# Kernel optimization log

Hardware: AMD Instinct MI355X
Metric: run time of the kernel (lower is better)

## Reference

```python
import jax, jax.numpy as jnp
import numpy as np
import math

B, WIN, C_IN, C_OUT = 8, 512, 38, 38
D_MODEL, N_HEADS, E_LAYERS, D_FF = 512, 8, 3, 512
EH = D_MODEL // N_HEADS
LN_EPS = 1e-3  # keras LayerNormalization default


def setup_inputs() -> dict:
    key = jax.random.key(0)
    ks = jax.random.split(key, 24)
    s = 0.02
    rn = lambda k, sh: jax.random.normal(k, sh, jnp.float32) * s
    L, d, H = E_LAYERS, D_MODEL, N_HEADS
    return {
        "x": jax.random.normal(ks[0], (B, WIN, C_IN), jnp.float32),
        "conv_k": rn(ks[1], (3, C_IN, d)),
        "Wq": rn(ks[2], (L, d, d)), "bq": jnp.zeros((L, d), jnp.float32),
        "Wk": rn(ks[3], (L, d, d)), "bk": jnp.zeros((L, d), jnp.float32),
        "Wv": rn(ks[4], (L, d, d)), "bv": jnp.zeros((L, d), jnp.float32),
        "Ws": rn(ks[5], (L, d, H)), "bs": jnp.zeros((L, H), jnp.float32),
        "Wo": rn(ks[6], (L, d, d)), "bo": jnp.zeros((L, d), jnp.float32),
        "W1": rn(ks[7], (L, d, D_FF)), "b1": jnp.zeros((L, D_FF), jnp.float32),
        "W2": rn(ks[8], (L, D_FF, d)), "b2": jnp.zeros((L, d), jnp.float32),
        "ln1_g": jnp.ones((L, d), jnp.float32), "ln1_b": jnp.zeros((L, d), jnp.float32),
        "ln2_g": jnp.ones((L, d), jnp.float32), "ln2_b": jnp.zeros((L, d), jnp.float32),
        "lnf_g": jnp.ones((d,), jnp.float32), "lnf_b": jnp.zeros((d,), jnp.float32),
        "Wp": rn(ks[9], (d, C_OUT)), "bp": jnp.zeros((C_OUT,), jnp.float32),
    }


def _layernorm(x, g, b):
    mu = jnp.mean(x, axis=-1, keepdims=True)
    var = jnp.mean((x - mu) ** 2, axis=-1, keepdims=True)
    return (x - mu) * jax.lax.rsqrt(var + LN_EPS) * g + b


def _pos_embedding():
    pos = jnp.arange(WIN, dtype=jnp.float32)[:, None]
    div = jnp.exp(jnp.arange(0, D_MODEL, 2, dtype=jnp.float32) * (-math.log(10000.0) / D_MODEL))
    # interleave sin at even idx, cos at odd idx
    return jnp.stack([jnp.sin(pos * div), jnp.cos(pos * div)], axis=-1).reshape(WIN, D_MODEL)


def reference(x, conv_k, Wq, bq, Wk, bk, Wv, bv, Ws, bs, Wo, bo,
              W1, b1, W2, b2, ln1_g, ln1_b, ln2_g, ln2_b, lnf_g, lnf_b, Wp, bp):
    # --- DataEmbedding: wrap-pad then Conv1D(k=3, valid), plus sinusoidal PE ---
    xp = jnp.concatenate([x[:, -1:], x, x[:, :1]], axis=1)
    h = jax.lax.conv_general_dilated(xp, conv_k, window_strides=(1,), padding='VALID',
                                     dimension_numbers=('NWC', 'WIO', 'NWC'))
    h = h + _pos_embedding()[None]

    idx = jnp.arange(WIN, dtype=jnp.float32)
    dist = jnp.abs(idx[:, None] - idx[None, :])
    scale = 1.0 / math.sqrt(EH)
    inv_sqrt_2pi = 1.0 / math.sqrt(2.0 * math.pi)

    series_l, prior_l, sigma_l = [], [], []
    for i in range(E_LAYERS):
        q = (h @ Wq[i] + bq[i]).reshape(B, WIN, N_HEADS, EH)
        k = (h @ Wk[i] + bk[i]).reshape(B, WIN, N_HEADS, EH)
        v = (h @ Wv[i] + bv[i]).reshape(B, WIN, N_HEADS, EH)
        sig = h @ Ws[i] + bs[i]

        scores = jnp.einsum('blhe,bshe->bhls', q, k)  # mask_flag=False in model
        series = jax.nn.softmax(scores * scale, axis=-1)  # [B, H, L, S]

        sg = jnp.transpose(sig, (0, 2, 1))               # [B, H, L]
        sg = jax.nn.sigmoid(sg * 5.0) + 1e-5
        sg = jnp.power(3.0, sg) - 1.0
        sg4 = jnp.broadcast_to(sg[..., None], (B, N_HEADS, WIN, WIN))
        prior = inv_sqrt_2pi / sg4 * jnp.exp(-(dist ** 2) / (2.0 * sg4 ** 2))

        attn_out = jnp.einsum('bhls,bshd->blhd', series, v).reshape(B, WIN, D_MODEL)
        h = _layernorm(h + attn_out @ Wo[i] + bo[i], ln1_g[i], ln1_b[i])
        y = jax.nn.gelu(h @ W1[i] + b1[i], approximate=False)
        y = y @ W2[i] + b2[i]
        h = _layernorm(h + y, ln2_g[i], ln2_b[i])

        series_l.append(series); prior_l.append(prior); sigma_l.append(sg4)

    h = _layernorm(h, lnf_g, lnf_b)
    out = h @ Wp + bp
    return (out, jnp.stack(series_l), jnp.stack(prior_l), jnp.stack(sigma_l))
```

## Files before the change

### kernel.cpp

```cpp
#include <hip/hip_runtime.h>
#include <math.h>


typedef unsigned short ushort;
typedef __attribute__((ext_vector_type(8))) ushort ushort8;
typedef __attribute__((ext_vector_type(8))) short short8;
typedef __attribute__((ext_vector_type(4))) float float4v;

__device__ inline ushort f2bf(float f) {
  union { float f; unsigned u; } v; v.f = f;
  return (ushort)((v.u + 0x7fffu + ((v.u >> 16) & 1u)) >> 16);
}

__device__ inline void gload16(const void* g, void* l) {
  __builtin_amdgcn_global_load_lds(
      (const __attribute__((address_space(1))) unsigned int*)g,
      (__attribute__((address_space(3))) unsigned int*)l, 16, 0, 0);
}

__global__ __launch_bounds__(512) void embed_kernel(const float* __restrict__ x,
                                                    const float* __restrict__ ck,
                                                    float* __restrict__ h,
                                                    ushort* __restrict__ hb) {
  int bt = blockIdx.x;
  int b = bt >> 9, t = bt & 511;
  int co = threadIdx.x;
  __shared__ float xs[3][38];
  if (co < 114) {
    int w = co / 38, ci = co - w * 38;
    int r = (t - 1 + w + 512) & 511;
    xs[w][ci] = x[((long)(b << 9) + r) * 38 + ci];
  }
  __syncthreads();
  float acc = 0.f;
#pragma unroll
  for (int w = 0; w < 3; ++w)
#pragma unroll
    for (int ci = 0; ci < 38; ++ci)
      acc = fmaf(xs[w][ci], ck[(w * 38 + ci) * 512 + co], acc);
  float div = expf((float)(co & ~1) * (-9.210340371976184f / 512.f));
  float ang = (float)t * div;
  float pe = (co & 1) ? cosf(ang) : sinf(ang);
  float o = acc + pe;
  h[(long)bt * 512 + co] = o;
  hb[(long)bt * 512 + co] = f2bf(o);
}

__global__ __launch_bounds__(256) void wcvt_kernel(const float* __restrict__ W,
                                                   ushort* __restrict__ Wt,
                                                   long lstride) {
  int l = blockIdx.z;
  int n = blockIdx.x * 256 + threadIdx.x;
  int k0 = blockIdx.y * 8;
  const float* w = W + (long)l * 262144;
  ushort* o = Wt + (long)l * lstride;
  ushort8 v;
#pragma unroll
  for (int i = 0; i < 8; ++i) v[i] = f2bf(w[(long)(k0 + i) * 512 + n]);
  *(ushort8*)&o[(long)n * 512 + k0] = v;
}

__global__ __launch_bounds__(512) void bcat_kernel(const float* __restrict__ bq,
                                                   const float* __restrict__ bk,
                                                   const float* __restrict__ bv,
                                                   float* __restrict__ bqkv) {
  int l = blockIdx.x, t = threadIdx.x;
  bqkv[l * 1536 + t] = bq[l * 512 + t];
  bqkv[l * 1536 + 512 + t] = bk[l * 512 + t];
  bqkv[l * 1536 + 1024 + t] = bv[l * 512 + t];
}

template <bool GELU_, bool CBF16>
__global__ __launch_bounds__(256) void gemm_bt(
    const ushort* __restrict__ A, int lda,
    const ushort* __restrict__ B, int ldb,
    const float* __restrict__ bias,
    void* __restrict__ Cv, int ldc, int K) {
  __shared__ ushort As[4096];
  __shared__ ushort Bs[2048];
  int t = threadIdx.x;
  int m0 = blockIdx.y * 128, n0 = blockIdx.x * 64;
  int w = t >> 6, lane = t & 63;
  int wr = (w >> 1) * 64, wc = (w & 1) * 32;
  int fm = lane & 15, q4 = lane >> 4;
  float4v acc[4][2];
#pragma unroll
  for (int i = 0; i < 4; ++i)
#pragma unroll
    for (int j = 0; j < 2; ++j) acc[i][j] = (float4v){0.f, 0.f, 0.f, 0.f};

  int kk = (lane & 3) * 8;
  const ushort* ga0 = &A[(long)(m0 + w * 32 + (lane >> 2)) * lda + kk];
  const ushort* ga1 = ga0 + (long)16 * lda;
  const ushort* gb = &B[(long)(n0 + w * 16 + (lane >> 2)) * ldb + kk];
  ushort* lA0 = &As[(w * 2) * 512];
  ushort* lA1 = &As[(w * 2 + 1) * 512];
  ushort* lB = &Bs[w * 512];

  for (int k0 = 0; k0 < K; k0 += 32) {
    gload16(ga0, lA0);
    gload16(ga1, lA1);
    gload16(gb, lB);
    ga0 += 32; ga1 += 32; gb += 32;
    __syncthreads();
    short8 a[4], bfr[2];
#pragma unroll
    for (int i = 0; i < 4; ++i)
      a[i] = *(const short8*)&As[(wr + 16 * i + fm) * 32 + q4 * 8];
#pragma unroll
    for (int j = 0; j < 2; ++j)
      bfr[j] = *(const short8*)&Bs[(wc + 16 * j + fm) * 32 + q4 * 8];
#pragma unroll
    for (int i = 0; i < 4; ++i)
#pragma unroll
      for (int j = 0; j < 2; ++j)
        acc[i][j] = __builtin_amdgcn_mfma_f32_16x16x32_bf16(a[i], bfr[j], acc[i][j], 0, 0, 0);
    __syncthreads();
  }

#pragma unroll
  for (int j = 0; j < 2; ++j) {
    int col = n0 + wc + 16 * j + fm;
    float bv = bias ? bias[col] : 0.f;
#pragma unroll
    for (int i = 0; i < 4; ++i) {
#pragma unroll
      for (int r = 0; r < 4; ++r) {
        int row = m0 + wr + 16 * i + q4 * 4 + r;
        float v = acc[i][j][r] + bv;
        if (GELU_) v = 0.5f * v * (1.f + erff(v * 0.7071067811865476f));
        if (CBF16)
          ((ushort*)Cv)[(long)row * ldc + col] = f2bf(v);
        else
          ((float*)Cv)[(long)row * ldc + col] = v;
      }
    }
  }
}

__global__ __launch_bounds__(256) void vtrans_kernel(const ushort* __restrict__ qkv,
                                                     ushort* __restrict__ vT) {
  int c = blockIdx.x, bh = blockIdx.y;
  int b = bh >> 3, hh = bh & 7;
  __shared__ ushort tile[64][72];
  int t = threadIdx.x;
  int sr = t >> 2, d0 = (t & 3) * 16;
  const ushort* src = &qkv[((long)b * 512 + c * 64 + sr) * 1536 + 1024 + hh * 64 + d0];
  *(ushort8*)&tile[sr][d0] = *(const ushort8*)src;
  *(ushort8*)&tile[sr][d0 + 8] = *(const ushort8*)(src + 8);
  __syncthreads();
  int d = t >> 2, s0 = (t & 3) * 16;
  ushort8 v0, v1;
#pragma unroll
  for (int e = 0; e < 8; ++e) {
    v0[e] = tile[s0 + e][d];
    v1[e] = tile[s0 + 8 + e][d];
  }
  ushort* dst = &vT[((long)bh * 64 + d) * 512 + c * 64 + s0];
  *(ushort8*)dst = v0;
  *(ushort8*)(dst + 8) = v1;
}

__global__ __launch_bounds__(256, 2) void attn_fused(
    const ushort* __restrict__ qkv, const ushort* __restrict__ vT,
    const float* __restrict__ sg,
    float* __restrict__ series, float* __restrict__ prior,
    float* __restrict__ sigma, ushort* __restrict__ t1b) {
  __shared__ ushort Ps[64 * 520];
  __shared__ float red[256];

  int t = threadIdx.x;
  int m0 = blockIdx.x * 64;
  int bh = blockIdx.y;
  int b = bh >> 3, hh = bh & 7;
  int w = t >> 6, lane = t & 63;
  int fm = lane & 15, q4 = lane >> 4;
  int wc = w * 128;
  long rowg = (long)b * 512;

  float4v acc[4][8];
#pragma unroll
  for (int i = 0; i < 4; ++i)
#pragma unroll
    for (int j = 0; j < 8; ++j) acc[i][j] = (float4v){0.f, 0.f, 0.f, 0.f};

  const ushort* qbase = &qkv[(rowg + m0) * 1536 + hh * 64];
  const ushort* kbase = &qkv[rowg * 1536 + 512 + hh * 64];
#pragma unroll
  for (int ks = 0; ks < 2; ++ks) {
    int ko = ks * 32 + q4 * 8;
    short8 a[4], bfr[8];
#pragma unroll
    for (int i = 0; i < 4; ++i)
      a[i] = *(const short8*)&qbase[(long)(16 * i + fm) * 1536 + ko];
#pragma unroll
    for (int j = 0; j < 8; ++j)
      bfr[j] = *(const short8*)&kbase[(long)(wc + 16 * j + fm) * 1536 + ko];
#pragma unroll
    for (int i = 0; i < 4; ++i)
#pragma unroll
      for (int j = 0; j < 8; ++j)
        acc[i][j] = __builtin_amdgcn_mfma_f32_16x16x32_bf16(a[i], bfr[j], acc[i][j], 0, 0, 0);
  }

#pragma unroll
  for (int i = 0; i < 4; ++i)
#pragma unroll
    for (int j = 0; j < 8; ++j)
#pragma unroll
      for (int r = 0; r < 4; ++r) acc[i][j][r] *= 0.125f;

  float mrow[4][4];
#pragma unroll
  for (int i = 0; i < 4; ++i)
#pragma unroll
    for (int r = 0; r < 4; ++r) {
      float m = acc[i][0][r];
#pragma unroll
      for (int j = 1; j < 8; ++j) m = fmaxf(m, acc[i][j][r]);
#pragma unroll
      for (int off = 1; off < 16; off <<= 1) m = fmaxf(m, __shfl_xor(m, off));
      mrow[i][r] = m;
    }
  if (fm == 0) {
#pragma unroll
    for (int i = 0; i < 4; ++i)
#pragma unroll
      for (int r = 0; r < 4; ++r)
        red[(16 * i + q4 * 4 + r) * 4 + w] = mrow[i][r];
  }
  __syncthreads();
#pragma unroll
  for (int i = 0; i < 4; ++i)
#pragma unroll
    for (int r = 0; r < 4; ++r) {
      const float* rp = &red[(16 * i + q4 * 4 + r) * 4];
      mrow[i][r] = fmaxf(fmaxf(rp[0], rp[1]), fmaxf(rp[2], rp[3]));
    }
  float lrow[4][4];
#pragma unroll
  for (int i = 0; i < 4; ++i)
#pragma unroll
    for (int r = 0; r < 4; ++r) {
      float s = 0.f;
#pragma unroll
      for (int j = 0; j < 8; ++j) {
        float e = __expf(acc[i][j][r] - mrow[i][r]);
        acc[i][j][r] = e;
        s += e;
      }
#pragma unroll
      for (int off = 1; off < 16; off <<= 1) s += __shfl_xor(s, off);
      lrow[i][r] = s;
    }
  __syncthreads();
  if (fm == 0) {
#pragma unroll
    for (int i = 0; i < 4; ++i)
#pragma unroll
      for (int r = 0; r < 4; ++r)
        red[(16 * i + q4 * 4 + r) * 4 + w] = lrow[i][r];
  }
  __syncthreads();
#pragma unroll
  for (int i = 0; i < 4; ++i)
#pragma unroll
    for (int r = 0; r < 4; ++r) {
      const float* rp = &red[(16 * i + q4 * 4 + r) * 4];
      lrow[i][r] = 1.f / (rp[0] + rp[1] + rp[2] + rp[3]);
    }

  float* serp = series + ((long)bh << 18);
#pragma unroll
  for (int i = 0; i < 4; ++i)
#pragma unroll
    for (int r = 0; r < 4; ++r) {
      int row = 16 * i + q4 * 4 + r;
      float inv = lrow[i][r];
#pragma unroll
      for (int j = 0; j < 8; ++j) {
        int col = wc + 16 * j + fm;
        float v = acc[i][j][r] * inv;
        serp[(long)(m0 + row) * 512 + col] = v;
        Ps[row * 520 + col] = f2bf(v);
      }
    }
  __syncthreads();

  float4v acc2[4] = {{0.f, 0.f, 0.f, 0.f}, {0.f, 0.f, 0.f, 0.f},
                     {0.f, 0.f, 0.f, 0.f}, {0.f, 0.f, 0.f, 0.f}};
  int wn = w * 16;
  const ushort* vbase = &vT[((long)bh * 64 + wn + fm) * 512];
#pragma unroll
  for (int c = 0; c < 8; ++c) {
#pragma unroll
    for (int ks = 0; ks < 2; ++ks) {
      int ko = ks * 32 + q4 * 8;
      short8 b2 = *(const short8*)&vbase[c * 64 + ko];
#pragma unroll
      for (int i = 0; i < 4; ++i) {
        short8 a2 = *(const short8*)&Ps[(16 * i + fm) * 520 + c * 64 + ko];
        acc2[i] = __builtin_amdgcn_mfma_f32_16x16x32_bf16(a2, b2, acc2[i], 0, 0, 0);
      }
    }
  }
#pragma unroll
  for (int i = 0; i < 4; ++i)
#pragma unroll
    for (int r = 0; r < 4; ++r)
      t1b[(rowg + m0 + 16 * i + q4 * 4 + r) * 512 + hh * 64 + wn + fm] =
          f2bf(acc2[i][r]);

  if (t < 64) {
    float xv = sg[(rowg + m0 + t) * 8 + hh];
    float s = 1.f / (1.f + __expf(-5.f * xv)) + 1e-5f;
    float sgv = expm1f(s * 1.0986122886681098f);
    red[t * 3] = sgv;
    red[t * 3 + 1] = 0.3989422804014327f / sgv;
    red[t * 3 + 2] = 1.f / sgv;
  }
  __syncthreads();
  float* prip = prior + ((long)bh << 18);
  float* sigp = sigma + ((long)bh << 18);
  for (int it = t; it < 8192; it += 256) {
    int row = it >> 7;
    int c4 = (it & 127) << 2;
    float sgv = red[row * 3], inv = red[row * 3 + 1], rinv = red[row * 3 + 2];
    float ig = (float)(m0 + row);
    float4 pv, sv;
#pragma unroll
    for (int e = 0; e < 4; ++e) {
      float dd = ig - (float)(c4 + e);
      float rr = dd * rinv;
      ((float*)&pv)[e] = inv * __expf(-0.5f * rr * rr);
      ((float*)&sv)[e] = sgv;
    }
    *(float4*)&prip[(long)(m0 + row) * 512 + c4] = pv;
    *(float4*)&sigp[(long)(m0 + row) * 512 + c4] = sv;
  }
}

__global__ __launch_bounds__(256) void ln_kernel(const float* __restrict__ x,
                                                 const float* __restrict__ delta,
                                                 const float* __restrict__ g,
                                                 const float* __restrict__ bb,
                                                 float* __restrict__ out,
                                                 ushort* __restrict__ hb) {
  long row = blockIdx.x;
  int tid = threadIdx.x;
  int c = tid * 2;
  float2 xv = *(const float2*)&x[row * 512 + c];
  if (delta) {
    float2 dv = *(const float2*)&delta[row * 512 + c];
    xv.x += dv.x; xv.y += dv.y;
  }
  float s = xv.x + xv.y;
  float q = xv.x * xv.x + xv.y * xv.y;
#pragma unroll
  for (int off = 1; off < 64; off <<= 1) {
    s += __shfl_xor(s, off);
    q += __shfl_xor(q, off);
  }
  __shared__ float red[8];
  int wid = tid >> 6;
  if ((tid & 63) == 0) { red[wid] = s; red[wid + 4] = q; }
  __syncthreads();
  float S = red[0] + red[1] + red[2] + red[3];
  float Q = red[4] + red[5] + red[6] + red[7];
  float mean = S * (1.f / 512.f);
  float var = Q * (1.f / 512.f) - mean * mean;
  float rstd = rsqrtf(var + 1e-3f);
  float2 o;
  o.x = (xv.x - mean) * rstd * g[c] + bb[c];
  o.y = (xv.y - mean) * rstd * g[c + 1] + bb[c + 1];
  *(float2*)&out[row * 512 + c] = o;
  if (hb) {
    unsigned pk = ((unsigned)f2bf(o.y) << 16) | (unsigned)f2bf(o.x);
    ((unsigned*)hb)[row * 256 + tid] = pk;
  }
}

template <int NOUT>
__global__ __launch_bounds__(256) void gemm_smallN(const float* __restrict__ A,
                                                   const float* __restrict__ W,
                                                   const float* __restrict__ bias,
                                                   float* __restrict__ C) {
  long row = (long)blockIdx.x * 4 + (threadIdx.x >> 6);
  int lane = threadIdx.x & 63;
  float acc[NOUT];
#pragma unroll
  for (int j = 0; j < NOUT; ++j) acc[j] = 0.f;
  for (int k = lane; k < 512; k += 64) {
    float a = A[row * 512 + k];
    const float* wr = W + (long)k * NOUT;
#pragma unroll
    for (int j = 0; j < NOUT; ++j) acc[j] = fmaf(a, wr[j], acc[j]);
  }
#pragma unroll
  for (int j = 0; j < NOUT; ++j)
#pragma unroll
    for (int off = 32; off; off >>= 1) acc[j] += __shfl_xor(acc[j], off);
  if (lane == 0) {
#pragma unroll
    for (int j = 0; j < NOUT; ++j) C[row * NOUT + j] = acc[j] + bias[j];
  }
}

extern "C" void kernel_launch(void* const* d_in, const int* in_sizes, int n_in,
                              void* d_out, int out_size, void* d_ws, size_t ws_size,
                              hipStream_t stream) {
  (void)in_sizes; (void)n_in; (void)out_size; (void)ws_size;
  const float* x    = (const float*)d_in[0];
  const float* ck   = (const float*)d_in[1];
  const float* Wq   = (const float*)d_in[2];
  const float* bq   = (const float*)d_in[3];
  const float* Wk   = (const float*)d_in[4];
  const float* bk   = (const float*)d_in[5];
  const float* Wv   = (const float*)d_in[6];
  const float* bv   = (const float*)d_in[7];
  const float* Wsw  = (const float*)d_in[8];
  const float* bsw  = (const float*)d_in[9];
  const float* Wo   = (const float*)d_in[10];
  const float* bo   = (const float*)d_in[11];
  const float* W1   = (const float*)d_in[12];
  const float* b1   = (const float*)d_in[13];
  const float* W2   = (const float*)d_in[14];
  const float* b2   = (const float*)d_in[15];
  const float* ln1g = (const float*)d_in[16];
  const float* ln1b = (const float*)d_in[17];
  const float* ln2g = (const float*)d_in[18];
  const float* ln2b = (const float*)d_in[19];
  const float* lnfg = (const float*)d_in[20];
  const float* lnfb = (const float*)d_in[21];
  const float* Wp   = (const float*)d_in[22];
  const float* bp   = (const float*)d_in[23];
  float* out = (float*)d_out;

  float* h    = (float*)d_ws;
  float* t1   = h + 2097152;
  float* t2   = t1 + 2097152;
  float* sg   = t2 + 2097152;
  float* bqkv = sg + 32768;
  ushort* qkv  = (ushort*)(bqkv + 4608);
  ushort* wqkv = qkv + 6291456;
  ushort* wo3  = wqkv + 2359296;
  ushort* w13  = wo3 + 786432;
  ushort* w23  = w13 + 786432;
  ushort* t1b = (ushort*)t1;
  ushort* hb  = (ushort*)(t1 + 1048576);
  ushort* vT  = (ushort*)t2;

  float* series0 = out + 155648;
  float* prior0  = out + 50487296;
  float* sigma0  = out + 100818944;

  dim3 gW(2, 64, 3);
  wcvt_kernel<<<gW, 256, 0, stream>>>(Wq, wqkv, 786432);
  wcvt_kernel<<<gW, 256, 0, stream>>>(Wk, wqkv + 262144, 786432);
  wcvt_kernel<<<gW, 256, 0, stream>>>(Wv, wqkv + 524288, 786432);
  wcvt_kernel<<<gW, 256, 0, stream>>>(Wo, wo3, 262144);
  wcvt_kernel<<<gW, 256, 0, stream>>>(W1, w13, 262144);
  wcvt_kernel<<<gW, 256, 0, stream>>>(W2, w23, 262144);
  bcat_kernel<<<3, 512, 0, stream>>>(bq, bk, bv, bqkv);

  embed_kernel<<<4096, 512, 0, stream>>>(x, ck, h, hb);

  dim3 gQKV(24, 32, 1);
  dim3 gFull(8, 32, 1);
  dim3 gVT(8, 64, 1);
  dim3 gAttn(8, 64, 1);

  for (int l = 0; l < 3; ++l) {
    float* ser = series0 + (long)l * 16777216;
    float* pri = prior0  + (long)l * 16777216;
    float* sgm = sigma0  + (long)l * 16777216;

    gemm_bt<false, true><<<gQKV, 256, 0, stream>>>(
        hb, 512, wqkv + (long)l * 786432, 512, bqkv + l * 1536, qkv, 1536, 512);
    gemm_smallN<8><<<1024, 256, 0, stream>>>(h, Wsw + (long)l * 4096, bsw + l * 8, sg);
    vtrans_kernel<<<gVT, 256, 0, stream>>>(qkv, vT);
    attn_fused<<<gAttn, 256, 0, stream>>>(qkv, vT, sg, ser, pri, sgm, t1b);
    gemm_bt<false, false><<<gFull, 256, 0, stream>>>(
        t1b, 512, wo3 + (long)l * 262144, 512, bo + (long)l * 512, t2, 512, 512);
    ln_kernel<<<4096, 256, 0, stream>>>(h, t2, ln1g + l * 512, ln1b + l * 512, h, hb);
    gemm_bt<true, true><<<gFull, 256, 0, stream>>>(
        hb, 512, w13 + (long)l * 262144, 512, b1 + (long)l * 512, t1b, 512, 512);
    gemm_bt<false, false><<<gFull, 256, 0, stream>>>(
        t1b, 512, w23 + (long)l * 262144, 512, b2 + (long)l * 512, t2, 512, 512);
    ln_kernel<<<4096, 256, 0, stream>>>(h, t2, ln2g + l * 512, ln2b + l * 512, h, hb);
  }

  ln_kernel<<<4096, 256, 0, stream>>>(h, nullptr, lnfg, lnfb, t1, nullptr);
  gemm_smallN<38><<<1024, 256, 0, stream>>>(t1, Wp, bp, out);
}
```

Measured before the change: 1.045 ms.

## Fuse V transpose into QKV GEMM, sigma projection into attention, double-buffer GEMM

The QKV GEMM epilogue now also writes V in transposed bf16 layout, which removes the separate vtrans kernel. The sigma projection (h @ Ws) moves into the attention kernel using a pre-transposed Ws, which removes the gemm_smallN launch per layer. Attention blocks shrink from 64 to 32 query rows, doubling the grid and halving the LDS footprint. The bf16 GEMM gets double-buffered LDS staging so global loads overlap MFMA work. In exchange, K rows are loaded twice as often by the smaller attention tiles, and the sigma dot product is recomputed for every query tile.

```diff
diff --git a/kernel.cpp b/kernel.cpp
--- a/kernel.cpp
+++ b/kernel.cpp
@@ -4,6 +4,7 @@
 
 typedef unsigned short ushort;
 typedef __attribute__((ext_vector_type(8))) ushort ushort8;
+typedef __attribute__((ext_vector_type(4))) ushort ushort4v;
 typedef __attribute__((ext_vector_type(8))) short short8;
 typedef __attribute__((ext_vector_type(4))) float float4v;
 
@@ -70,14 +71,23 @@
   bqkv[l * 1536 + 1024 + t] = bv[l * 512 + t];
 }
 
-template <bool GELU_, bool CBF16>
+__global__ __launch_bounds__(512) void wst_kernel(const float* __restrict__ Ws,
+                                                  float* __restrict__ WsT) {
+  int l = blockIdx.x, k = threadIdx.x;
+#pragma unroll
+  for (int hh = 0; hh < 8; ++hh)
+    WsT[(long)l * 4096 + hh * 512 + k] = Ws[(long)l * 4096 + k * 8 + hh];
+}
+
+template <bool GELU_, bool CBF16, bool VST>
 __global__ __launch_bounds__(256) void gemm_bt(
     const ushort* __restrict__ A, int lda,
     const ushort* __restrict__ B, int ldb,
     const float* __restrict__ bias,
-    void* __restrict__ Cv, int ldc, int K) {
-  __shared__ ushort As[4096];
-  __shared__ ushort Bs[2048];
+    void* __restrict__ Cv, int ldc, int K,
+    ushort* __restrict__ vTout) {
+  __shared__ ushort As[2][4096];
+  __shared__ ushort Bs[2][2048];
   int t = threadIdx.x;
   int m0 = blockIdx.y * 128, n0 = blockIdx.x * 64;
   int w = t >> 6, lane = t & 63;
@@ -93,28 +103,37 @@
   const ushort* ga0 = &A[(long)(m0 + w * 32 + (lane >> 2)) * lda + kk];
   const ushort* ga1 = ga0 + (long)16 * lda;
   const ushort* gb = &B[(long)(n0 + w * 16 + (lane >> 2)) * ldb + kk];
-  ushort* lA0 = &As[(w * 2) * 512];
-  ushort* lA1 = &As[(w * 2 + 1) * 512];
-  ushort* lB = &Bs[w * 512];
-
-  for (int k0 = 0; k0 < K; k0 += 32) {
-    gload16(ga0, lA0);
-    gload16(ga1, lA1);
-    gload16(gb, lB);
+
+  auto stage = [&](int bi) {
+    gload16(ga0, &As[bi][w * 1024]);
+    gload16(ga1, &As[bi][w * 1024 + 512]);
+    gload16(gb, &Bs[bi][w * 512]);
     ga0 += 32; ga1 += 32; gb += 32;
-    __syncthreads();
+  };
+  auto compute = [&](int bi) {
     short8 a[4], bfr[2];
 #pragma unroll
     for (int i = 0; i < 4; ++i)
-      a[i] = *(const short8*)&As[(wr + 16 * i + fm) * 32 + q4 * 8];
+      a[i] = *(const short8*)&As[bi][(wr + 16 * i + fm) * 32 + q4 * 8];
 #pragma unroll
     for (int j = 0; j < 2; ++j)
-      bfr[j] = *(const short8*)&Bs[(wc + 16 * j + fm) * 32 + q4 * 8];
+      bfr[j] = *(const short8*)&Bs[bi][(wc + 16 * j + fm) * 32 + q4 * 8];
 #pragma unroll
     for (int i = 0; i < 4; ++i)
 #pragma unroll
       for (int j = 0; j < 2; ++j)
         acc[i][j] = __builtin_amdgcn_mfma_f32_16x16x32_bf16(a[i], bfr[j], acc[i][j], 0, 0, 0);
+  };
+
+  stage(0);
+  __syncthreads();
+#pragma unroll 1
+  for (int k0 = 0; k0 < K; k0 += 64) {
+    stage(1);
+    compute(0);
+    __syncthreads();
+    if (k0 + 64 < K) stage(0);
+    compute(1);
     __syncthreads();
   }
 
@@ -124,53 +143,43 @@
     float bv = bias ? bias[col] : 0.f;
 #pragma unroll
     for (int i = 0; i < 4; ++i) {
+      int row0 = m0 + wr + 16 * i + q4 * 4;
+      float vv[4];
 #pragma unroll
       for (int r = 0; r < 4; ++r) {
-        int row = m0 + wr + 16 * i + q4 * 4 + r;
         float v = acc[i][j][r] + bv;
         if (GELU_) v = 0.5f * v * (1.f + erff(v * 0.7071067811865476f));
+        vv[r] = v;
         if (CBF16)
-          ((ushort*)Cv)[(long)row * ldc + col] = f2bf(v);
+          ((ushort*)Cv)[(long)(row0 + r) * ldc + col] = f2bf(v);
         else
-          ((float*)Cv)[(long)row * ldc + col] = v;
+          ((float*)Cv)[(long)(row0 + r) * ldc + col] = v;
       }
-    }
-  }
-}
-
-__global__ __launch_bounds__(256) void vtrans_kernel(const ushort* __restrict__ qkv,
-                                                     ushort* __restrict__ vT) {
-  int c = blockIdx.x, bh = blockIdx.y;
-  int b = bh >> 3, hh = bh & 7;
-  __shared__ ushort tile[64][72];
-  int t = threadIdx.x;
-  int sr = t >> 2, d0 = (t & 3) * 16;
-  const ushort* src = &qkv[((long)b * 512 + c * 64 + sr) * 1536 + 1024 + hh * 64 + d0];
-  *(ushort8*)&tile[sr][d0] = *(const ushort8*)src;
-  *(ushort8*)&tile[sr][d0 + 8] = *(const ushort8*)(src + 8);
-  __syncthreads();
-  int d = t >> 2, s0 = (t & 3) * 16;
-  ushort8 v0, v1;
-#pragma unroll
-  for (int e = 0; e < 8; ++e) {
-    v0[e] = tile[s0 + e][d];
-    v1[e] = tile[s0 + 8 + e][d];
-  }
-  ushort* dst = &vT[((long)bh * 64 + d) * 512 + c * 64 + s0];
-  *(ushort8*)dst = v0;
-  *(ushort8*)(dst + 8) = v1;
+      if (VST && n0 >= 1024) {
+        int d = (col - 1024) & 63;
+        int hh = (n0 - 1024) >> 6;
+        int bb = row0 >> 9, s0 = row0 & 511;
+        ushort4v pk;
+#pragma unroll
+        for (int r = 0; r < 4; ++r) pk[r] = f2bf(vv[r]);
+        *(ushort4v*)&vTout[((long)(bb * 8 + hh) * 64 + d) * 512 + s0] = pk;
+      }
+    }
+  }
 }
 
 __global__ __launch_bounds__(256, 2) void attn_fused(
     const ushort* __restrict__ qkv, const ushort* __restrict__ vT,
-    const float* __restrict__ sg,
+    const float* __restrict__ h, const float* __restrict__ WsT,
+    const float* __restrict__ bsw,
     float* __restrict__ series, float* __restrict__ prior,
     float* __restrict__ sigma, ushort* __restrict__ t1b) {
-  __shared__ ushort Ps[64 * 520];
-  __shared__ float red[256];
+  __shared__ ushort Ps[32 * 520];
+  __shared__ float red[128];
+  __shared__ float sgc[96];
 
   int t = threadIdx.x;
-  int m0 = blockIdx.x * 64;
+  int m0 = blockIdx.x * 32;
   int bh = blockIdx.y;
   int b = bh >> 3, hh = bh & 7;
   int w = t >> 6, lane = t & 63;
@@ -178,9 +187,31 @@
   int wc = w * 128;
   long rowg = (long)b * 512;
 
-  float4v acc[4][8];
-#pragma unroll
-  for (int i = 0; i < 4; ++i)
+  {
+    int r = t >> 3, p = t & 7;
+    const float* hrow = &h[(rowg + m0 + r) * 512 + p * 64];
+    const float* wcol = &WsT[hh * 512 + p * 64];
+    float s = 0.f;
+#pragma unroll
+    for (int i = 0; i < 16; ++i) {
+      float4 hv = *(const float4*)&hrow[i * 4];
+      float4 wv = *(const float4*)&wcol[i * 4];
+      s += hv.x * wv.x + hv.y * wv.y + hv.z * wv.z + hv.w * wv.w;
+    }
+    s += __shfl_xor(s, 1); s += __shfl_xor(s, 2); s += __shfl_xor(s, 4);
+    if (p == 0) {
+      float xv = s + bsw[hh];
+      float sig = 1.f / (1.f + __expf(-5.f * xv)) + 1e-5f;
+      float sgv = expm1f(sig * 1.0986122886681098f);
+      sgc[r * 3] = sgv;
+      sgc[r * 3 + 1] = 0.3989422804014327f / sgv;
+      sgc[r * 3 + 2] = 1.f / sgv;
+    }
+  }
+
+  float4v acc[2][8];
+#pragma unroll
+  for (int i = 0; i < 2; ++i)
 #pragma unroll
     for (int j = 0; j < 8; ++j) acc[i][j] = (float4v){0.f, 0.f, 0.f, 0.f};
 
@@ -189,30 +220,30 @@
 #pragma unroll
   for (int ks = 0; ks < 2; ++ks) {
     int ko = ks * 32 + q4 * 8;
-    short8 a[4], bfr[8];
-#pragma unroll
-    for (int i = 0; i < 4; ++i)
+    short8 a[2], bfr[8];
+#pragma unroll
+    for (int i = 0; i < 2; ++i)
       a[i] = *(const short8*)&qbase[(long)(16 * i + fm) * 1536 + ko];
 #pragma unroll
     for (int j = 0; j < 8; ++j)
       bfr[j] = *(const short8*)&kbase[(long)(wc + 16 * j + fm) * 1536 + ko];
 #pragma unroll
-    for (int i = 0; i < 4; ++i)
+    for (int i = 0; i < 2; ++i)
 #pragma unroll
       for (int j = 0; j < 8; ++j)
         acc[i][j] = __builtin_amdgcn_mfma_f32_16x16x32_bf16(a[i], bfr[j], acc[i][j], 0, 0, 0);
   }
 
 #pragma unroll
-  for (int i = 0; i < 4; ++i)
+  for (int i = 0; i < 2; ++i)
 #pragma unroll
     for (int j = 0; j < 8; ++j)
 #pragma unroll
       for (int r = 0; r < 4; ++r) acc[i][j][r] *= 0.125f;
 
-  float mrow[4][4];
-#pragma unroll
-  for (int i = 0; i < 4; ++i)
+  float mrow[2][4];
+#pragma unroll
+  for (int i = 0; i < 2; ++i)
 #pragma unroll
     for (int r = 0; r < 4; ++r) {
       float m = acc[i][0][r];
@@ -224,22 +255,22 @@
     }
   if (fm == 0) {
 #pragma unroll
-    for (int i = 0; i < 4; ++i)
+    for (int i = 0; i < 2; ++i)
 #pragma unroll
       for (int r = 0; r < 4; ++r)
         red[(16 * i + q4 * 4 + r) * 4 + w] = mrow[i][r];
   }
   __syncthreads();
 #pragma unroll
-  for (int i = 0; i < 4; ++i)
+  for (int i = 0; i < 2; ++i)
 #pragma unroll
     for (int r = 0; r < 4; ++r) {
       const float* rp = &red[(16 * i + q4 * 4 + r) * 4];
       mrow[i][r] = fmaxf(fmaxf(rp[0], rp[1]), fmaxf(rp[2], rp[3]));
     }
-  float lrow[4][4];
-#pragma unroll
-  for (int i = 0; i < 4; ++i)
+  float lrow[2][4];
+#pragma unroll
+  for (int i = 0; i < 2; ++i)
 #pragma unroll
     for (int r = 0; r < 4; ++r) {
       float s = 0.f;
@@ -256,14 +287,14 @@
   __syncthreads();
   if (fm == 0) {
 #pragma unroll
-    for (int i = 0; i < 4; ++i)
+    for (int i = 0; i < 2; ++i)
 #pragma unroll
       for (int r = 0; r < 4; ++r)
         red[(16 * i + q4 * 4 + r) * 4 + w] = lrow[i][r];
   }
   __syncthreads();
 #pragma unroll
-  for (int i = 0; i < 4; ++i)
+  for (int i = 0; i < 2; ++i)
 #pragma unroll
     for (int r = 0; r < 4; ++r) {
       const float* rp = &red[(16 * i + q4 * 4 + r) * 4];
@@ -272,7 +303,7 @@
 
   float* serp = series + ((long)bh << 18);
 #pragma unroll
-  for (int i = 0; i < 4; ++i)
+  for (int i = 0; i < 2; ++i)
 #pragma unroll
     for (int r = 0; r < 4; ++r) {
       int row = 16 * i + q4 * 4 + r;
@@ -287,8 +318,7 @@
     }
   __syncthreads();
 
-  float4v acc2[4] = {{0.f, 0.f, 0.f, 0.f}, {0.f, 0.f, 0.f, 0.f},
-                     {0.f, 0.f, 0.f, 0.f}, {0.f, 0.f, 0.f, 0.f}};
+  float4v acc2[2] = {{0.f, 0.f, 0.f, 0.f}, {0.f, 0.f, 0.f, 0.f}};
   int wn = w * 16;
   const ushort* vbase = &vT[((long)bh * 64 + wn + fm) * 512];
 #pragma unroll
@@ -298,34 +328,25 @@
       int ko = ks * 32 + q4 * 8;
       short8 b2 = *(const short8*)&vbase[c * 64 + ko];
 #pragma unroll
-      for (int i = 0; i < 4; ++i) {
+      for (int i = 0; i < 2; ++i) {
         short8 a2 = *(const short8*)&Ps[(16 * i + fm) * 520 + c * 64 + ko];
         acc2[i] = __builtin_amdgcn_mfma_f32_16x16x32_bf16(a2, b2, acc2[i], 0, 0, 0);
       }
     }
   }
 #pragma unroll
-  for (int i = 0; i < 4; ++i)
+  for (int i = 0; i < 2; ++i)
 #pragma unroll
     for (int r = 0; r < 4; ++r)
       t1b[(rowg + m0 + 16 * i + q4 * 4 + r) * 512 + hh * 64 + wn + fm] =
           f2bf(acc2[i][r]);
 
-  if (t < 64) {
-    float xv = sg[(rowg + m0 + t) * 8 + hh];
-    float s = 1.f / (1.f + __expf(-5.f * xv)) + 1e-5f;
-    float sgv = expm1f(s * 1.0986122886681098f);
-    red[t * 3] = sgv;
-    red[t * 3 + 1] = 0.3989422804014327f / sgv;
-    red[t * 3 + 2] = 1.f / sgv;
-  }
-  __syncthreads();
   float* prip = prior + ((long)bh << 18);
   float* sigp = sigma + ((long)bh << 18);
-  for (int it = t; it < 8192; it += 256) {
+  for (int it = t; it < 4096; it += 256) {
     int row = it >> 7;
     int c4 = (it & 127) << 2;
-    float sgv = red[row * 3], inv = red[row * 3 + 1], rinv = red[row * 3 + 2];
+    float sgv = sgc[row * 3], inv = sgc[row * 3 + 1], rinv = sgc[row * 3 + 2];
     float ig = (float)(m0 + row);
     float4 pv, sv;
 #pragma unroll
@@ -439,8 +460,8 @@
   float* h    = (float*)d_ws;
   float* t1   = h + 2097152;
   float* t2   = t1 + 2097152;
-  float* sg   = t2 + 2097152;
-  float* bqkv = sg + 32768;
+  float* wst  = t2 + 2097152;
+  float* bqkv = wst + 32768;
   ushort* qkv  = (ushort*)(bqkv + 4608);
   ushort* wqkv = qkv + 6291456;
   ushort* wo3  = wqkv + 2359296;
@@ -462,31 +483,30 @@
   wcvt_kernel<<<gW, 256, 0, stream>>>(W1, w13, 262144);
   wcvt_kernel<<<gW, 256, 0, stream>>>(W2, w23, 262144);
   bcat_kernel<<<3, 512, 0, stream>>>(bq, bk, bv, bqkv);
+  wst_kernel<<<3, 512, 0, stream>>>(Wsw, wst);
 
   embed_kernel<<<4096, 512, 0, stream>>>(x, ck, h, hb);
 
   dim3 gQKV(24, 32, 1);
   dim3 gFull(8, 32, 1);
-  dim3 gVT(8, 64, 1);
-  dim3 gAttn(8, 64, 1);
+  dim3 gAttn(16, 64, 1);
 
   for (int l = 0; l < 3; ++l) {
     float* ser = series0 + (long)l * 16777216;
     float* pri = prior0  + (long)l * 16777216;
     float* sgm = sigma0  + (long)l * 16777216;
 
-    gemm_bt<false, true><<<gQKV, 256, 0, stream>>>(
-        hb, 512, wqkv + (long)l * 786432, 512, bqkv + l * 1536, qkv, 1536, 512);
-    gemm_smallN<8><<<1024, 256, 0, stream>>>(h, Wsw + (long)l * 4096, bsw + l * 8, sg);
-    vtrans_kernel<<<gVT, 256, 0, stream>>>(qkv, vT);
-    attn_fused<<<gAttn, 256, 0, stream>>>(qkv, vT, sg, ser, pri, sgm, t1b);
-    gemm_bt<false, false><<<gFull, 256, 0, stream>>>(
-        t1b, 512, wo3 + (long)l * 262144, 512, bo + (long)l * 512, t2, 512, 512);
+    gemm_bt<false, true, true><<<gQKV, 256, 0, stream>>>(
+        hb, 512, wqkv + (long)l * 786432, 512, bqkv + l * 1536, qkv, 1536, 512, vT);
+    attn_fused<<<gAttn, 256, 0, stream>>>(qkv, vT, h, wst + (long)l * 4096,
+                                          bsw + (long)l * 8, ser, pri, sgm, t1b);
+    gemm_bt<false, false, false><<<gFull, 256, 0, stream>>>(
+        t1b, 512, wo3 + (long)l * 262144, 512, bo + (long)l * 512, t2, 512, 512, nullptr);
     ln_kernel<<<4096, 256, 0, stream>>>(h, t2, ln1g + l * 512, ln1b + l * 512, h, hb);
-    gemm_bt<true, true><<<gFull, 256, 0, stream>>>(
-        hb, 512, w13 + (long)l * 262144, 512, b1 + (long)l * 512, t1b, 512, 512);
-    gemm_bt<false, false><<<gFull, 256, 0, stream>>>(
-        t1b, 512, w23 + (long)l * 262144, 512, b2 + (long)l * 512, t2, 512, 512);
+    gemm_bt<true, true, false><<<gFull, 256, 0, stream>>>(
+        hb, 512, w13 + (long)l * 262144, 512, b1 + (long)l * 512, t1b, 512, 512, nullptr);
+    gemm_bt<false, false, false><<<gFull, 256, 0, stream>>>(
+        t1b, 512, w23 + (long)l * 262144, 512, b2 + (long)l * 512, t2, 512, 512, nullptr);
     ln_kernel<<<4096, 256, 0, stream>>>(h, t2, ln2g + l * 512, ln2b + l * 512, h, hb);
   }
 
```

Measured after the change: 1.037 ms. No clear change (-0.7%).
